# Optimization experiments

Hardware: AMD Instinct MI355X
Metric: run time of the kernel (lower is better)

The kernel has to match this reference:

```python
import jax, jax.numpy as jnp
import numpy as np

SEQ_LEN = 1024
BATCH = 256
HIDDEN = 100
OUT = 1

L_FILTER = [-0.0106, 0.0329, 0.0308, -0.187, -0.028, 0.6309, 0.7148, 0.2304]
H_FILTER = [-0.2304, 0.7148, -0.6309, -0.028, 0.187, 0.0308, -0.0329, -0.0106]


def _create_W(P, is_l, rng):
    filt = L_FILTER if is_l else H_FILTER
    eps = np.min(np.abs(filt))
    W = rng.standard_normal((P, P)) * 0.1 * eps
    for i in range(P):
        for k, j in enumerate(range(i, min(i + len(filt), P))):
            W[i, j] = filt[k]
    return jnp.asarray(W, dtype=jnp.float32)


def setup_inputs() -> dict:
    key = jax.random.key(0)
    ks = jax.random.split(key, 16)
    rng = np.random.default_rng(0)
    T, H = SEQ_LEN, HIDDEN
    s = 1.0 / np.sqrt(H)

    def lstm_params(k):
        k1, k2, k3 = jax.random.split(k, 3)
        Wih = jax.random.uniform(k1, (4 * H, 1), jnp.float32, -s, s)
        Whh = jax.random.uniform(k2, (4 * H, H), jnp.float32, -s, s)
        b = jax.random.uniform(k3, (4 * H,), jnp.float32, -s, s)
        return Wih, Whh, b

    Wih1, Whh1, b1 = lstm_params(ks[0])
    Wih2, Whh2, b2 = lstm_params(ks[1])
    Wih3, Whh3, b3 = lstm_params(ks[2])
    return {
        "x": jax.random.normal(ks[3], (BATCH, T, 1), jnp.float32),
        "W1H": _create_W(T, False, rng),
        "b1H": jax.random.uniform(ks[4], (T,), jnp.float32, -1 / np.sqrt(T), 1 / np.sqrt(T)),
        "W1L": _create_W(T, True, rng),
        "b1L": jax.random.uniform(ks[5], (T,), jnp.float32, -1 / np.sqrt(T), 1 / np.sqrt(T)),
        "W2H": _create_W(T // 2, False, rng),
        "b2H": jax.random.uniform(ks[6], (T // 2,), jnp.float32, -1 / np.sqrt(T // 2), 1 / np.sqrt(T // 2)),
        "W2L": _create_W(T // 2, True, rng),
        "b2L": jax.random.uniform(ks[7], (T // 2,), jnp.float32, -1 / np.sqrt(T // 2), 1 / np.sqrt(T // 2)),
        "Wih1": Wih1, "Whh1": Whh1, "b1": b1,
        "Wih2": Wih2, "Whh2": Whh2, "b2": b2,
        "Wih3": Wih3, "Whh3": Whh3, "b3": b3,
        "Wout": jax.random.uniform(ks[8], (OUT, H), jnp.float32, -s, s),
        "bout": jax.random.uniform(ks[9], (OUT,), jnp.float32, -s, s),
    }


def _avgpool2(x):  # [B, L] -> [B, L//2], AvgPool1d(kernel=2, stride=2)
    B, L = x.shape
    return x.reshape(B, L // 2, 2).mean(-1)


def _lstm(x, Wih, Whh, b):
    # x: [B, T, 1]; torch LSTM gate order i, f, g, o; h0 = c0 = 0
    H = Whh.shape[1]
    gx = jnp.einsum('bti,gi->btg', x, Wih) + b  # [B, T, 4H]

    def step(carry, g):
        h, c = carry
        z = g + h @ Whh.T
        i, f, gg, o = jnp.split(z, 4, axis=-1)
        c = jax.nn.sigmoid(f) * c + jax.nn.sigmoid(i) * jnp.tanh(gg)
        h = jax.nn.sigmoid(o) * jnp.tanh(c)
        return (h, c), h

    B = x.shape[0]
    h0 = jnp.zeros((B, H), x.dtype)
    _, hs = jax.lax.scan(step, (h0, h0), jnp.swapaxes(gx, 0, 1))
    return jnp.swapaxes(hs, 0, 1)  # [B, T, H]


def reference(x, W1H, b1H, W1L, b1L, W2H, b2H, W2L, b2L,
              Wih1, Whh1, b1, Wih2, Whh2, b2, Wih3, Whh3, b3, Wout, bout):
    inp = x[:, :, -1]  # [B, T]
    ah1 = jax.nn.sigmoid(inp @ W1H.T + b1H)
    al1 = jax.nn.sigmoid(inp @ W1L.T + b1L)
    xh1 = _avgpool2(ah1)  # [B, T/2]
    xl1 = _avgpool2(al1)  # [B, T/2]
    ah2 = jax.nn.sigmoid(xl1 @ W2H.T + b2H)
    al2 = jax.nn.sigmoid(xl1 @ W2L.T + b2L)
    xh2 = _avgpool2(ah2)  # [B, T/4]
    xl2 = _avgpool2(al2)  # [B, T/4]
    s1 = _lstm(xh1[..., None], Wih1, Whh1, b1)
    s2 = _lstm(xh2[..., None], Wih2, Whh2, b2)
    s3 = _lstm(xl2[..., None], Wih3, Whh3, b3)
    cat = jnp.concatenate([s1, s2, s3], axis=1)  # [B, T, H]
    out = cat @ Wout.T + bout  # [B, T, OUT]
    return out[:, -1, :]
```

## Files before the change

### kernel.cpp

```cpp
#include <hip/hip_runtime.h>
#include <math.h>

typedef __bf16 bf16x8 __attribute__((ext_vector_type(8)));
typedef float f32x4 __attribute__((ext_vector_type(4)));

__device__ __forceinline__ unsigned short f2bf(float f) {
  unsigned int u = __builtin_bit_cast(unsigned int, f);
  u += 0x7fffu + ((u >> 16) & 1u);
  return (unsigned short)(u >> 16);
}
__device__ __forceinline__ unsigned int pack2bf(float a, float b) {
  return (unsigned int)f2bf(a) | ((unsigned int)f2bf(b) << 16);
}

#define GK_PADK 40
template <int WFP32, int XFP32>
__global__ __launch_bounds__(256) void gemm_mfma_sig_pool(
    const void* __restrict__ Wv, const float* __restrict__ bias,
    const void* __restrict__ Xv, void* __restrict__ Y,
    int K, int Np, int out_bf16) {
  __shared__ unsigned short Wt[64][GK_PADK];
  __shared__ unsigned short Xt[64][GK_PADK];
  const int tid = threadIdx.x;
  const int i_base = blockIdx.x * 64;
  const int b_base = blockIdx.y * 64;
  const int srow = tid >> 2, sseg = tid & 3;
  const int wv = tid >> 6, lane = tid & 63;
  const int wn = wv & 1, wb = wv >> 1;
  const int L15 = lane & 15, q = lane >> 4;

  f32x4 acc[2][2] = {};
  for (int k0 = 0; k0 < K; k0 += 32) {
    if (WFP32) {
      const float* Wf = (const float*)Wv;
      const float4 a = *(const float4*)&Wf[(size_t)(i_base + srow) * K + k0 + sseg * 8];
      const float4 b = *(const float4*)&Wf[(size_t)(i_base + srow) * K + k0 + sseg * 8 + 4];
      uint4 p = { pack2bf(a.x, a.y), pack2bf(a.z, a.w), pack2bf(b.x, b.y), pack2bf(b.z, b.w) };
      *(uint4*)&Wt[srow][sseg * 8] = p;
    } else {
      *(uint4*)&Wt[srow][sseg * 8] =
          *(const uint4*)&((const unsigned short*)Wv)[(size_t)(i_base + srow) * K + k0 + sseg * 8];
    }
    if (XFP32) {
      const float* Xf = (const float*)Xv;
      const float4 a = *(const float4*)&Xf[(size_t)(b_base + srow) * K + k0 + sseg * 8];
      const float4 b = *(const float4*)&Xf[(size_t)(b_base + srow) * K + k0 + sseg * 8 + 4];
      uint4 p = { pack2bf(a.x, a.y), pack2bf(a.z, a.w), pack2bf(b.x, b.y), pack2bf(b.z, b.w) };
      *(uint4*)&Xt[srow][sseg * 8] = p;
    } else {
      *(uint4*)&Xt[srow][sseg * 8] =
          *(const uint4*)&((const unsigned short*)Xv)[(size_t)(b_base + srow) * K + k0 + sseg * 8];
    }
    __syncthreads();
    bf16x8 a0 = *(const bf16x8*)&Wt[wn * 32 + L15][q * 8];
    bf16x8 a1 = *(const bf16x8*)&Wt[wn * 32 + 16 + L15][q * 8];
    bf16x8 b0 = *(const bf16x8*)&Xt[wb * 32 + L15][q * 8];
    bf16x8 b1 = *(const bf16x8*)&Xt[wb * 32 + 16 + L15][q * 8];
    acc[0][0] = __builtin_amdgcn_mfma_f32_16x16x32_bf16(a0, b0, acc[0][0], 0, 0, 0);
    acc[0][1] = __builtin_amdgcn_mfma_f32_16x16x32_bf16(a0, b1, acc[0][1], 0, 0, 0);
    acc[1][0] = __builtin_amdgcn_mfma_f32_16x16x32_bf16(a1, b0, acc[1][0], 0, 0, 0);
    acc[1][1] = __builtin_amdgcn_mfma_f32_16x16x32_bf16(a1, b1, acc[1][1], 0, 0, 0);
    __syncthreads();
  }

  const int nb0 = i_base + wn * 32;
  const int bc0 = b_base + wb * 32 + L15;
#pragma unroll
  for (int mg = 0; mg < 2; mg++) {
    const int nrow = nb0 + mg * 16 + q * 4;
    const float bi0 = bias[nrow], bi1 = bias[nrow + 1];
    const float bi2 = bias[nrow + 2], bi3 = bias[nrow + 3];
#pragma unroll
    for (int bg = 0; bg < 2; bg++) {
      const int b = bc0 + bg * 16;
      f32x4 A = acc[mg][bg];
      const float a0 = __builtin_amdgcn_rcpf(1.f + __expf(-(A[0] + bi0)));
      const float a1 = __builtin_amdgcn_rcpf(1.f + __expf(-(A[1] + bi1)));
      const float a2 = __builtin_amdgcn_rcpf(1.f + __expf(-(A[2] + bi2)));
      const float a3 = __builtin_amdgcn_rcpf(1.f + __expf(-(A[3] + bi3)));
      const float p0 = 0.5f * (a0 + a1), p1 = 0.5f * (a2 + a3);
      const int pidx = nrow >> 1;
      if (out_bf16) {
        *(unsigned int*)&((unsigned short*)Y)[(size_t)b * Np + pidx] = pack2bf(p0, p1);
      } else {
        *(float2*)&((float*)Y)[(size_t)b * Np + pidx] = make_float2(p0, p1);
      }
    }
  }
}

#define HID 100
#define TSTEPS 256
#define LTHREADS 832
#define HSTRIDE 36

__device__ __forceinline__ float qx1(float x) {
  int v = __builtin_amdgcn_mov_dpp(__builtin_bit_cast(int, x), 0xB1, 0xf, 0xf, true);
  return x + __builtin_bit_cast(float, v);
}
__device__ __forceinline__ float qx2(float x) {
  int v = __builtin_amdgcn_mov_dpp(__builtin_bit_cast(int, x), 0x4E, 0xf, 0xf, true);
  return x + __builtin_bit_cast(float, v);
}

__global__ __launch_bounds__(LTHREADS) __attribute__((amdgpu_waves_per_eu(1, 4)))
void lstm_tail(
    const float* __restrict__ X, const float* __restrict__ Wih,
    const float* __restrict__ Whh, const float* __restrict__ bgates,
    const float* __restrict__ Wout, const float* __restrict__ bout,
    float* __restrict__ out) {
  const int bat = blockIdx.x;
  const int t = threadIdx.x;
  const int r = t >> 3;
  const int gp = (t >> 2) & 1;
  const int kq = t & 3;
  const bool wvalid = (r < HID);
  const int rr = wvalid ? r : 0;
  const int rowA = gp * 200 + rr;
  const int rowB = rowA + 100;
  const int koff = 25 * kq;

  __shared__ __align__(16) float hbuf[2][160];
  __shared__ float zs[400];
  __shared__ float xrow[TSTEPS];
  __shared__ float red[HID];

  for (int i = t; i < TSTEPS; i += LTHREADS) xrow[i] = X[(size_t)bat * TSTEPS + i];

  const float* WA = &Whh[(size_t)rowA * HID + koff];
  const float* WB = &Whh[(size_t)rowB * HID + koff];
#define DECLW(P) float4 P##_0, P##_1, P##_2, P##_3, P##_4, P##_5; float P##_6;
  DECLW(wa) DECLW(wb)
#undef DECLW
#define LW(P, B)                                      \
  P##_0 = make_float4(B[0],  B[1],  B[2],  B[3]);     \
  P##_1 = make_float4(B[4],  B[5],  B[6],  B[7]);     \
  P##_2 = make_float4(B[8],  B[9],  B[10], B[11]);    \
  P##_3 = make_float4(B[12], B[13], B[14], B[15]);    \
  P##_4 = make_float4(B[16], B[17], B[18], B[19]);    \
  P##_5 = make_float4(B[20], B[21], B[22], B[23]);    \
  P##_6 = B[24];
  LW(wa, WA) LW(wb, WB)
#undef LW

  const bool doact = wvalid && (kq == 1 || kq == 2);
  const int wrow = (kq == 1) ? rowA : rowB;
  const float u_  = Wih[wrow];
  const float bz_ = bgates[wrow];
  const bool is_tanh = (kq == 1 && gp == 1);
  const float ka = is_tanh ? 2.f : 1.f;
  const float ma = is_tanh ? 2.f : 1.f;
  const float da = is_tanh ? -1.f : 0.f;

  if (t < 160) { hbuf[0][t] = 0.f; hbuf[1][t] = 0.f; }
  float c = 0.f;
  __syncthreads();

  for (int step = 0; step < TSTEPS; step++) {
    const int cur = step & 1;
    const float* hq = &hbuf[cur][kq * HSTRIDE];
    float za = 0.f, zb = 0.f;
#define DG(OFF, A, B)                                        \
    { const float4 h4 = *(const float4*)&hq[OFF];            \
      za = fmaf(A.x, h4.x, za); zb = fmaf(B.x, h4.x, zb);    \
      za = fmaf(A.y, h4.y, za); zb = fmaf(B.y, h4.y, zb);    \
      za = fmaf(A.z, h4.z, za); zb = fmaf(B.z, h4.z, zb);    \
      za = fmaf(A.w, h4.w, za); zb = fmaf(B.w, h4.w, zb); }
    DG(0,  wa_0, wb_0)
    DG(4,  wa_1, wb_1)
    DG(8,  wa_2, wb_2)
    DG(12, wa_3, wb_3)
    DG(16, wa_4, wb_4)
    DG(20, wa_5, wb_5)
    { const float h1 = hq[24];
      za = fmaf(wa_6, h1, za); zb = fmaf(wb_6, h1, zb); }
#undef DG
    za = qx2(qx1(za));
    zb = qx2(qx1(zb));
    if (doact) {
      const float zsel = (kq == 1) ? za : zb;
      const float zfull = fmaf(u_, xrow[step], zsel + bz_);
      zs[wrow] = ma * __builtin_amdgcn_rcpf(1.f + __expf(-ka * zfull)) + da;
    }
    __syncthreads();
    if (t < HID) {
      const float ai = zs[t], af = zs[t + 100], ag = zs[t + 200], ao = zs[t + 300];
      c = fmaf(af, c, ai * ag);
      const float th = 2.f * __builtin_amdgcn_rcpf(1.f + __expf(-2.f * c)) - 1.f;
      hbuf[cur ^ 1][(t / 25) * HSTRIDE + (t % 25)] = ao * th;
    }
    __syncthreads();
  }

  if (t < HID) red[t] = hbuf[0][(t / 25) * HSTRIDE + (t % 25)] * Wout[t];
  __syncthreads();
  if (t == 0) {
    float s = 0.f;
#pragma unroll
    for (int k = 0; k < HID; k++) s += red[k];
    out[bat] = s + bout[0];
  }
}

extern "C" void kernel_launch(void* const* d_in, const int* in_sizes, int n_in,
                              void* d_out, int out_size, void* d_ws, size_t ws_size,
                              hipStream_t stream) {
  const float* x    = (const float*)d_in[0];
  const float* W1L  = (const float*)d_in[3];
  const float* b1L  = (const float*)d_in[4];
  const float* W2L  = (const float*)d_in[7];
  const float* b2L  = (const float*)d_in[8];
  const float* Wih3 = (const float*)d_in[15];
  const float* Whh3 = (const float*)d_in[16];
  const float* b3   = (const float*)d_in[17];
  const float* Wout = (const float*)d_in[18];
  const float* bout = (const float*)d_in[19];
  float* out = (float*)d_out;

  unsigned short* xl1b = (unsigned short*)d_ws;
  float* xl2 = (float*)(xl1b + (size_t)256 * 512);

  gemm_mfma_sig_pool<1, 1><<<dim3(16, 4), 256, 0, stream>>>(W1L, b1L, x, xl1b, 1024, 512, 1);
  gemm_mfma_sig_pool<1, 0><<<dim3(8, 4), 256, 0, stream>>>(W2L, b2L, xl1b, xl2, 512, 256, 0);
  lstm_tail<<<256, LTHREADS, 0, stream>>>(xl2, Wih3, Whh3, b3, Wout, bout, out);
}
```

Baseline: 286.6 us.

## Use fp16 dot2 recurrence and swizzle gate exchange to drop a barrier per step

The LSTM recurrence now stores weights and hidden state as packed fp16 pairs and accumulates with the fdot2 instruction, which halves the register and LDS footprint of the matvec. Gate preactivations are exchanged between lane groups with a ds_swizzle instead of going through shared memory. Every lane then computes the cell update redundantly, so only one __syncthreads per timestep remains instead of two. The cost is reduced precision in the weights and hidden state, which could change the output of a 256-step recurrence.

New measurement: 327.6 us. +14.3%, slower.

```diff
diff --git a/kernel.cpp b/kernel.cpp
--- a/kernel.cpp
+++ b/kernel.cpp
@@ -3,6 +3,7 @@
 
 typedef __bf16 bf16x8 __attribute__((ext_vector_type(8)));
 typedef float f32x4 __attribute__((ext_vector_type(4)));
+typedef _Float16 h2 __attribute__((ext_vector_type(2)));
 
 __device__ __forceinline__ unsigned short f2bf(float f) {
   unsigned int u = __builtin_bit_cast(unsigned int, f);
@@ -92,7 +93,16 @@
 #define HID 100
 #define TSTEPS 256
 #define LTHREADS 832
-#define HSTRIDE 36
+
+#if __has_builtin(__builtin_amdgcn_fdot2)
+#define FDOT(a, b, c) __builtin_amdgcn_fdot2((a), (b), (c), false)
+#else
+__device__ __forceinline__ float FDOT(h2 a, h2 b, float c) {
+  c = fmaf((float)a.x, (float)b.x, c);
+  c = fmaf((float)a.y, (float)b.y, c);
+  return c;
+}
+#endif
 
 __device__ __forceinline__ float qx1(float x) {
   int v = __builtin_amdgcn_mov_dpp(__builtin_bit_cast(int, x), 0xB1, 0xf, 0xf, true);
@@ -102,9 +112,12 @@
   int v = __builtin_amdgcn_mov_dpp(__builtin_bit_cast(int, x), 0x4E, 0xf, 0xf, true);
   return x + __builtin_bit_cast(float, v);
 }
-
-__global__ __launch_bounds__(LTHREADS) __attribute__((amdgpu_waves_per_eu(1, 4)))
-void lstm_tail(
+__device__ __forceinline__ float swz4(float x) {
+  int v = __builtin_amdgcn_ds_swizzle(__builtin_bit_cast(int, x), 0x101F);
+  return __builtin_bit_cast(float, v);
+}
+
+__global__ __launch_bounds__(LTHREADS) void lstm_tail(
     const float* __restrict__ X, const float* __restrict__ Wih,
     const float* __restrict__ Whh, const float* __restrict__ bgates,
     const float* __restrict__ Wout, const float* __restrict__ bout,
@@ -114,85 +127,77 @@
   const int r = t >> 3;
   const int gp = (t >> 2) & 1;
   const int kq = t & 3;
-  const bool wvalid = (r < HID);
-  const int rr = wvalid ? r : 0;
+  const bool valid = (r < HID);
+  const int rr = valid ? r : 0;
   const int rowA = gp * 200 + rr;
   const int rowB = rowA + 100;
-  const int koff = 25 * kq;
-
-  __shared__ __align__(16) float hbuf[2][160];
-  __shared__ float zs[400];
+
+  __shared__ __align__(16) h2 hbuf[2][64];
   __shared__ float xrow[TSTEPS];
   __shared__ float red[HID];
 
   for (int i = t; i < TSTEPS; i += LTHREADS) xrow[i] = X[(size_t)bat * TSTEPS + i];
-
-  const float* WA = &Whh[(size_t)rowA * HID + koff];
-  const float* WB = &Whh[(size_t)rowB * HID + koff];
-#define DECLW(P) float4 P##_0, P##_1, P##_2, P##_3, P##_4, P##_5; float P##_6;
+  if (t < 64) { hbuf[0][t] = (h2){(_Float16)0.f, (_Float16)0.f};
+                hbuf[1][t] = (h2){(_Float16)0.f, (_Float16)0.f}; }
+
+#define DECLW(P) h2 P##_0, P##_1, P##_2, P##_3, P##_4, P##_5, P##_6, \
+                    P##_7, P##_8, P##_9, P##_10, P##_11, P##_12;
   DECLW(wa) DECLW(wb)
 #undef DECLW
-#define LW(P, B)                                      \
-  P##_0 = make_float4(B[0],  B[1],  B[2],  B[3]);     \
-  P##_1 = make_float4(B[4],  B[5],  B[6],  B[7]);     \
-  P##_2 = make_float4(B[8],  B[9],  B[10], B[11]);    \
-  P##_3 = make_float4(B[12], B[13], B[14], B[15]);    \
-  P##_4 = make_float4(B[16], B[17], B[18], B[19]);    \
-  P##_5 = make_float4(B[20], B[21], B[22], B[23]);    \
-  P##_6 = B[24];
-  LW(wa, WA) LW(wb, WB)
-#undef LW
-
-  const bool doact = wvalid && (kq == 1 || kq == 2);
-  const int wrow = (kq == 1) ? rowA : rowB;
-  const float u_  = Wih[wrow];
-  const float bz_ = bgates[wrow];
-  const bool is_tanh = (kq == 1 && gp == 1);
-  const float ka = is_tanh ? 2.f : 1.f;
-  const float ma = is_tanh ? 2.f : 1.f;
-  const float da = is_tanh ? -1.f : 0.f;
-
-  if (t < 160) { hbuf[0][t] = 0.f; hbuf[1][t] = 0.f; }
+#define LOADP(m)                                                              \
+  { const int p = kq + 4 * (m);                                               \
+    float fx = 0.f, fy = 0.f, gx = 0.f, gy = 0.f;                             \
+    if (p <= 49) {                                                            \
+      const float2 va = *(const float2*)&Whh[(size_t)rowA * HID + 2 * p];     \
+      const float2 vb = *(const float2*)&Whh[(size_t)rowB * HID + 2 * p];     \
+      fx = va.x; fy = va.y; gx = vb.x; gy = vb.y;                             \
+    }                                                                         \
+    wa_##m = (h2){(_Float16)fx, (_Float16)fy};                                \
+    wb_##m = (h2){(_Float16)gx, (_Float16)gy}; }
+  LOADP(0) LOADP(1) LOADP(2) LOADP(3) LOADP(4) LOADP(5) LOADP(6)
+  LOADP(7) LOADP(8) LOADP(9) LOADP(10) LOADP(11) LOADP(12)
+#undef LOADP
+
+  const float bA = bgates[rowA], bB = bgates[rowB];
+  const float uA = Wih[rowA],    uB = Wih[rowB];
   float c = 0.f;
   __syncthreads();
 
   for (int step = 0; step < TSTEPS; step++) {
     const int cur = step & 1;
-    const float* hq = &hbuf[cur][kq * HSTRIDE];
+    const h2* hq = &hbuf[cur][0];
     float za = 0.f, zb = 0.f;
-#define DG(OFF, A, B)                                        \
-    { const float4 h4 = *(const float4*)&hq[OFF];            \
-      za = fmaf(A.x, h4.x, za); zb = fmaf(B.x, h4.x, zb);    \
-      za = fmaf(A.y, h4.y, za); zb = fmaf(B.y, h4.y, zb);    \
-      za = fmaf(A.z, h4.z, za); zb = fmaf(B.z, h4.z, zb);    \
-      za = fmaf(A.w, h4.w, za); zb = fmaf(B.w, h4.w, zb); }
-    DG(0,  wa_0, wb_0)
-    DG(4,  wa_1, wb_1)
-    DG(8,  wa_2, wb_2)
-    DG(12, wa_3, wb_3)
-    DG(16, wa_4, wb_4)
-    DG(20, wa_5, wb_5)
-    { const float h1 = hq[24];
-      za = fmaf(wa_6, h1, za); zb = fmaf(wb_6, h1, zb); }
-#undef DG
+#define DOTP(m)                                   \
+    { const h2 hp = hq[kq + 4 * (m)];             \
+      za = FDOT(wa_##m, hp, za);                  \
+      zb = FDOT(wb_##m, hp, zb); }
+    DOTP(0) DOTP(1) DOTP(2) DOTP(3) DOTP(4) DOTP(5) DOTP(6)
+    DOTP(7) DOTP(8) DOTP(9) DOTP(10) DOTP(11) DOTP(12)
+#undef DOTP
     za = qx2(qx1(za));
     zb = qx2(qx1(zb));
-    if (doact) {
-      const float zsel = (kq == 1) ? za : zb;
-      const float zfull = fmaf(u_, xrow[step], zsel + bz_);
-      zs[wrow] = ma * __builtin_amdgcn_rcpf(1.f + __expf(-ka * zfull)) + da;
+    const float xt = xrow[step];
+    za += fmaf(uA, xt, bA);
+    zb += fmaf(uB, xt, bB);
+    const float oza = swz4(za), ozb = swz4(zb);
+    const float zi = gp ? oza : za;
+    const float zf = gp ? ozb : zb;
+    const float zg = gp ? za : oza;
+    const float zo = gp ? zb : ozb;
+    const float ai = __builtin_amdgcn_rcpf(1.f + __expf(-zi));
+    const float af = __builtin_amdgcn_rcpf(1.f + __expf(-zf));
+    const float ag = 2.f * __builtin_amdgcn_rcpf(1.f + __expf(-2.f * zg)) - 1.f;
+    const float ao = __builtin_amdgcn_rcpf(1.f + __expf(-zo));
+    c = fmaf(af, c, ai * ag);
+    const float th = 2.f * __builtin_amdgcn_rcpf(1.f + __expf(-2.f * c)) - 1.f;
+    const float h = ao * th;
+    if (((t & 7) == 0) && valid) {
+      ((_Float16*)&hbuf[cur ^ 1][0])[r] = (_Float16)h;
     }
     __syncthreads();
-    if (t < HID) {
-      const float ai = zs[t], af = zs[t + 100], ag = zs[t + 200], ao = zs[t + 300];
-      c = fmaf(af, c, ai * ag);
-      const float th = 2.f * __builtin_amdgcn_rcpf(1.f + __expf(-2.f * c)) - 1.f;
-      hbuf[cur ^ 1][(t / 25) * HSTRIDE + (t % 25)] = ao * th;
-    }
-    __syncthreads();
-  }
-
-  if (t < HID) red[t] = hbuf[0][(t / 25) * HSTRIDE + (t % 25)] * Wout[t];
+  }
+
+  if (t < HID) red[t] = (float)((const _Float16*)&hbuf[0][0])[t] * Wout[t];
   __syncthreads();
   if (t == 0) {
     float s = 0.f;
```
